# Kernel optimization log

Hardware: AMD Instinct MI355X
Metric: run time of the kernel (lower is better)

The kernel has to match this reference:

```python
import jax, jax.numpy as jnp
import numpy as np

B, N, K, D = 64, 1024, 512, 256  # batch, positions, codes, H*W


def setup_inputs() -> dict:
    key = jax.random.key(0)
    k1, k2 = jax.random.split(key)
    z_e_x = jax.random.normal(k1, (B, N, D), dtype=jnp.float32)
    # nn.Embedding(K, H*W) initialized uniform(-1/K, 1/K)
    codebook = jax.random.uniform(k2, (K, D), dtype=jnp.float32,
                                  minval=-1.0 / K, maxval=1.0 / K)
    return {"z_e_x": z_e_x, "codebook": codebook}


def _nearest_code(flat, codebook):
    # squared L2 distance via expansion: ||z||^2 - 2 z.e + ||e||^2
    d = ((flat * flat).sum(-1, keepdims=True)
         - 2.0 * flat @ codebook.T
         + (codebook * codebook).sum(-1))  # [M, K]
    return jnp.argmin(d, axis=-1)  # [M]


def reference(z_e_x, codebook):
    # Faithful to VQEmbedding.straight_through(z_e_x):
    #   z_q_x: quantized with straight-through estimator (grad -> z_e_x)
    #   z_q_x_bar: gather from live codebook (grad -> codebook)
    flat = z_e_x.reshape(-1, codebook.shape[1])  # [M, D]
    idx = _nearest_code(flat, jax.lax.stop_gradient(codebook))
    cb_sg = jax.lax.stop_gradient(codebook)
    z_q_st = flat + jax.lax.stop_gradient(cb_sg[idx] - flat)
    z_q_x = z_q_st.reshape(z_e_x.shape)
    z_q_x_bar = codebook[idx].reshape(z_e_x.shape)
    return z_q_x, z_q_x_bar
```

## Files before the change

### kernel.cpp

```cpp
#include <hip/hip_runtime.h>
#include <math.h>
#include <limits.h>

#define M_ROWS 65536
#define DD     256
#define KC     512
#define RPW    8
#define RPB    32

__device__ __forceinline__ float pw128_sq(const float4* __restrict__ q) {
  float r[8];
  {
    float4 a = q[0], b = q[1];
    r[0] = __fmul_rn(a.x, a.x); r[1] = __fmul_rn(a.y, a.y);
    r[2] = __fmul_rn(a.z, a.z); r[3] = __fmul_rn(a.w, a.w);
    r[4] = __fmul_rn(b.x, b.x); r[5] = __fmul_rn(b.y, b.y);
    r[6] = __fmul_rn(b.z, b.z); r[7] = __fmul_rn(b.w, b.w);
  }
#pragma unroll
  for (int i = 2; i < 32; i += 2) {
    float4 a = q[i], b = q[i + 1];
    r[0] = __fadd_rn(r[0], __fmul_rn(a.x, a.x));
    r[1] = __fadd_rn(r[1], __fmul_rn(a.y, a.y));
    r[2] = __fadd_rn(r[2], __fmul_rn(a.z, a.z));
    r[3] = __fadd_rn(r[3], __fmul_rn(a.w, a.w));
    r[4] = __fadd_rn(r[4], __fmul_rn(b.x, b.x));
    r[5] = __fadd_rn(r[5], __fmul_rn(b.y, b.y));
    r[6] = __fadd_rn(r[6], __fmul_rn(b.z, b.z));
    r[7] = __fadd_rn(r[7], __fmul_rn(b.w, b.w));
  }
  return __fadd_rn(__fadd_rn(__fadd_rn(r[0], r[1]), __fadd_rn(r[2], r[3])),
                   __fadd_rn(__fadd_rn(r[4], r[5]), __fadd_rn(r[6], r[7])));
}

__global__ void sumsq_kernel(const float* __restrict__ x, float* __restrict__ s,
                             int nrows) {
  int r = blockIdx.x * blockDim.x + threadIdx.x;
  if (r >= nrows) return;
  const float4* q = (const float4*)(x + (size_t)r * DD);
  s[r] = __fadd_rn(pw128_sq(q), pw128_sq(q + 32));
}

typedef __attribute__((address_space(1))) const void gas_void;
typedef __attribute__((address_space(3))) void las_void;
__device__ __forceinline__ void gl_lds16(const void* g, void* l) {
  __builtin_amdgcn_global_load_lds((gas_void*)g, (las_void*)l, 16, 0, 0);
}

__global__ __launch_bounds__(256) void vq_kernel(
    const float* __restrict__ z, const float* __restrict__ cb,
    const float* __restrict__ s, const float* __restrict__ se,
    float* __restrict__ out) {
  __shared__ float4 es4[KC * 4];
  __shared__ int best_l[RPB];

  const int tid = threadIdx.x;
  const int lane = tid & 63;
  const int wv = tid >> 6;
  const int rowbase =
      __builtin_amdgcn_readfirstlane((int)blockIdx.x * RPB + wv * RPW);
  const float4* zq = (const float4*)(z + (size_t)rowbase * DD);
  const float4* cg = (const float4*)cb;
  const int esw = (lane >> 1) & 3;

  float se_reg[8];
#pragma unroll
  for (int j = 0; j < 8; ++j) se_reg[j] = se[lane + 64 * j];

  float acc[8][8];
#pragma unroll
  for (int i = 0; i < 8; ++i)
#pragma unroll
    for (int j = 0; j < 8; ++j) acc[i][j] = 0.0f;

#pragma unroll 1
  for (int ks = 0; ks < 16; ++ks) {
#pragma unroll
    for (int seg = 0; seg < 8; ++seg) {
      int u = (wv * 8 + seg) * 64 + lane;
      int c = u >> 2;
      int q = (u & 3) ^ ((c >> 1) & 3);
      gl_lds16(&cg[(size_t)c * 64 + ks * 4 + q],
               (char*)es4 + (wv * 8 + seg) * 1024);
    }
    __syncthreads();

#pragma unroll
    for (int k4 = 0; k4 < 4; ++k4) {
      const float4* ep = &es4[lane * 4 + (k4 ^ esw)];
      float4 ef[8];
#pragma unroll
      for (int j = 0; j < 8; ++j) ef[j] = ep[j * 256];
#pragma unroll
      for (int i = 0; i < 8; ++i) {
        float4 zf = zq[(size_t)i * 64 + ks * 4 + k4];
#pragma unroll
        for (int j = 0; j < 8; ++j) {
          acc[i][j] = __fmaf_rn(zf.x, ef[j].x, acc[i][j]);
          acc[i][j] = __fmaf_rn(zf.y, ef[j].y, acc[i][j]);
          acc[i][j] = __fmaf_rn(zf.z, ef[j].z, acc[i][j]);
          acc[i][j] = __fmaf_rn(zf.w, ef[j].w, acc[i][j]);
        }
      }
    }
    __syncthreads();
  }

#pragma unroll
  for (int i = 0; i < 8; ++i) {
    float s_r = s[rowbase + i];
    float bd = INFINITY;
    int   bi = INT_MAX;
#pragma unroll
    for (int j = 0; j < 8; ++j) {
      int code = lane + 64 * j;
      float d = __fadd_rn(__fsub_rn(s_r, __fmul_rn(2.0f, acc[i][j])),
                          se_reg[j]);
      if (d < bd || (d == bd && code < bi)) { bd = d; bi = code; }
    }
#pragma unroll
    for (int off = 1; off < 64; off <<= 1) {
      float od = __shfl_xor(bd, off, 64);
      int   oi = __shfl_xor(bi, off, 64);
      if (od < bd || (od == bd && oi < bi)) { bd = od; bi = oi; }
    }
    if (lane == 0) best_l[wv * RPW + i] = bi;
  }
  __syncthreads();

  const int r0 = blockIdx.x * RPB;
  const float4* zg = (const float4*)z;
  float4* out0 = (float4*)out;
  float4* out1 = (float4*)(out + (size_t)M_ROWS * DD);
#pragma unroll
  for (int it = 0; it < 8; ++it) {
    int row = it * 4 + wv;
    size_t gidx = (size_t)(r0 + row) * 64 + lane;
    float4 zv = zg[gidx];
    float4 cv = cg[(size_t)best_l[row] * 64 + lane];
    float4 o0;
    o0.x = __fadd_rn(zv.x, __fsub_rn(cv.x, zv.x));
    o0.y = __fadd_rn(zv.y, __fsub_rn(cv.y, zv.y));
    o0.z = __fadd_rn(zv.z, __fsub_rn(cv.z, zv.z));
    o0.w = __fadd_rn(zv.w, __fsub_rn(cv.w, zv.w));
    out0[gidx] = o0;
    out1[gidx] = cv;
  }
}

extern "C" void kernel_launch(void* const* d_in, const int* in_sizes, int n_in,
                              void* d_out, int out_size, void* d_ws, size_t ws_size,
                              hipStream_t stream) {
  const float* z  = (const float*)d_in[0];
  const float* cb = (const float*)d_in[1];
  float* out = (float*)d_out;
  float* s  = (float*)d_ws;
  float* se = s + M_ROWS;

  sumsq_kernel<<<M_ROWS / 256, 256, 0, stream>>>(z, s, M_ROWS);
  sumsq_kernel<<<KC / 256, 256, 0, stream>>>(cb, se, KC);
  vq_kernel<<<M_ROWS / RPB, 256, 0, stream>>>(z, cb, s, se, out);
}
```

Measured before the change: 303.1 us.

## Double-buffer codebook LDS tiles and enlarge per-wave row tile in VQ kernel

Restructures the distance GEMM so each block has 8 waves of 16 rows each (128 rows per block) and stages codebook slices of 32 floats into double-buffered LDS. The next slice is loaded asynchronously while the current one is computed, which removes one barrier per step. Larger per-wave tiles cut codebook LDS traffic per FMA. The cost is higher register pressure (128 accumulators per lane) and 128 KB of LDS per block, which can lower occupancy and risks spills.

```diff
diff --git a/kernel.cpp b/kernel.cpp
--- a/kernel.cpp
+++ b/kernel.cpp
@@ -5,8 +5,10 @@
 #define M_ROWS 65536
 #define DD     256
 #define KC     512
-#define RPW    8
-#define RPB    32
+#define RPW    16
+#define WAVES  8
+#define RPB    (RPW * WAVES)
+#define KS     32
 
 __device__ __forceinline__ float pw128_sq(const float4* __restrict__ q) {
   float r[8];
@@ -47,11 +49,11 @@
   __builtin_amdgcn_global_load_lds((gas_void*)g, (las_void*)l, 16, 0, 0);
 }
 
-__global__ __launch_bounds__(256) void vq_kernel(
+__global__ __launch_bounds__(512) void vq_kernel(
     const float* __restrict__ z, const float* __restrict__ cb,
     const float* __restrict__ s, const float* __restrict__ se,
     float* __restrict__ out) {
-  __shared__ float4 es4[KC * 4];
+  __shared__ float4 es4[2][KC * 8];
   __shared__ int best_l[RPB];
 
   const int tid = threadIdx.x;
@@ -61,39 +63,39 @@
       __builtin_amdgcn_readfirstlane((int)blockIdx.x * RPB + wv * RPW);
   const float4* zq = (const float4*)(z + (size_t)rowbase * DD);
   const float4* cg = (const float4*)cb;
-  const int esw = (lane >> 1) & 3;
+  const int esw = lane & 7;
 
   float se_reg[8];
 #pragma unroll
   for (int j = 0; j < 8; ++j) se_reg[j] = se[lane + 64 * j];
 
-  float acc[8][8];
+  float acc[RPW][8];
 #pragma unroll
-  for (int i = 0; i < 8; ++i)
+  for (int i = 0; i < RPW; ++i)
 #pragma unroll
     for (int j = 0; j < 8; ++j) acc[i][j] = 0.0f;
 
-#pragma unroll 1
-  for (int ks = 0; ks < 16; ++ks) {
+  auto stage = [&](int b, int ks) {
 #pragma unroll
     for (int seg = 0; seg < 8; ++seg) {
-      int u = (wv * 8 + seg) * 64 + lane;
-      int c = u >> 2;
-      int q = (u & 3) ^ ((c >> 1) & 3);
-      gl_lds16(&cg[(size_t)c * 64 + ks * 4 + q],
-               (char*)es4 + (wv * 8 + seg) * 1024);
+      int u = seg * 512 + tid;
+      int c = u >> 3, qs = u & 7;
+      int q = qs ^ (c & 7);
+      gl_lds16(&cg[(size_t)c * 64 + ks * 8 + q],
+               (char*)&es4[b][0] + (size_t)(seg * 512 + wv * 64) * 16);
     }
-    __syncthreads();
+  };
 
+  auto compute = [&](int b, int ks) {
 #pragma unroll
-    for (int k4 = 0; k4 < 4; ++k4) {
-      const float4* ep = &es4[lane * 4 + (k4 ^ esw)];
+    for (int k4 = 0; k4 < 8; ++k4) {
+      const float4* ep = &es4[b][lane * 8 + (k4 ^ esw)];
       float4 ef[8];
 #pragma unroll
-      for (int j = 0; j < 8; ++j) ef[j] = ep[j * 256];
+      for (int j = 0; j < 8; ++j) ef[j] = ep[j * 512];
 #pragma unroll
-      for (int i = 0; i < 8; ++i) {
-        float4 zf = zq[(size_t)i * 64 + ks * 4 + k4];
+      for (int i = 0; i < RPW; ++i) {
+        float4 zf = zq[(size_t)i * 64 + ks * 8 + k4];
 #pragma unroll
         for (int j = 0; j < 8; ++j) {
           acc[i][j] = __fmaf_rn(zf.x, ef[j].x, acc[i][j]);
@@ -103,11 +105,21 @@
         }
       }
     }
+  };
+
+  stage(0, 0);
+  __syncthreads();
+  int b = 0;
+#pragma unroll 1
+  for (int ks = 0; ks < DD / KS; ++ks) {
+    if (ks < DD / KS - 1) stage(b ^ 1, ks + 1);
+    compute(b, ks);
     __syncthreads();
+    b ^= 1;
   }
 
 #pragma unroll
-  for (int i = 0; i < 8; ++i) {
+  for (int i = 0; i < RPW; ++i) {
     float s_r = s[rowbase + i];
     float bd = INFINITY;
     int   bi = INT_MAX;
@@ -133,11 +145,12 @@
   float4* out0 = (float4*)out;
   float4* out1 = (float4*)(out + (size_t)M_ROWS * DD);
 #pragma unroll
-  for (int it = 0; it < 8; ++it) {
-    int row = it * 4 + wv;
-    size_t gidx = (size_t)(r0 + row) * 64 + lane;
+  for (int it = 0; it < (RPB * 64) / 512; ++it) {
+    int u = it * 512 + tid;
+    int row = u >> 6, c4 = u & 63;
+    size_t gidx = (size_t)(r0 + row) * 64 + c4;
     float4 zv = zg[gidx];
-    float4 cv = cg[(size_t)best_l[row] * 64 + lane];
+    float4 cv = cg[(size_t)best_l[row] * 64 + c4];
     float4 o0;
     o0.x = __fadd_rn(zv.x, __fsub_rn(cv.x, zv.x));
     o0.y = __fadd_rn(zv.y, __fsub_rn(cv.y, zv.y));
@@ -159,5 +172,5 @@
 
   sumsq_kernel<<<M_ROWS / 256, 256, 0, stream>>>(z, s, M_ROWS);
   sumsq_kernel<<<KC / 256, 256, 0, stream>>>(cb, se, KC);
-  vq_kernel<<<M_ROWS / RPB, 256, 0, stream>>>(z, cb, s, se, out);
+  vq_kernel<<<M_ROWS / RPB, 512, 0, stream>>>(z, cb, s, se, out);
 }
```

Measured after the change: 425.3 us. 40.3% more time.

## Prefilter nearest codes with bf16 MFMA, then rescore candidates in fp32

Applied to the files above, without the earlier changes.

Replaces the single fp32 FMA distance kernel with a two-stage search. A bf16 MFMA pass computes approximate distances (the codebook norm is folded in as an extra K-slice) and keeps every code within an error-bound threshold of the row minimum. A second kernel rescores up to 32 candidates per row exactly in fp32, falling back to a full scan when more survive. This moves the bulk of the distance arithmetic onto matrix cores, at the cost of extra launches, a candidate buffer, and reliance on a heuristic threshold to keep exact argmin semantics.

```diff
diff --git a/kernel.cpp b/kernel.cpp
--- a/kernel.cpp
+++ b/kernel.cpp
@@ -5,8 +5,15 @@
 #define M_ROWS 65536
 #define DD     256
 #define KC     512
-#define RPW    8
-#define RPB    32
+#define CAP    32
+
+typedef __attribute__((ext_vector_type(8))) short bf16x8;
+typedef __attribute__((ext_vector_type(4))) float f32x4;
+
+__device__ __forceinline__ unsigned short bf16rne(float f) {
+  unsigned u = __float_as_uint(f);
+  return (unsigned short)((u + 0x7FFFu + ((u >> 16) & 1u)) >> 16);
+}
 
 __device__ __forceinline__ float pw128_sq(const float4* __restrict__ q) {
   float r[8];
@@ -47,105 +54,191 @@
   __builtin_amdgcn_global_load_lds((gas_void*)g, (las_void*)l, 16, 0, 0);
 }
 
-__global__ __launch_bounds__(256) void vq_kernel(
+__global__ void build_img_kernel(const float* __restrict__ cb,
+                                 const float* __restrict__ se,
+                                 unsigned short* __restrict__ img) {
+  int u0 = blockIdx.x * 256 + threadIdx.x;
+  if (u0 >= 9 * KC * 4) return;
+  int x = u0 & 3, c = (u0 >> 2) & (KC - 1), s = u0 >> 11;
+  int u = x ^ ((c >> 1) & 3);
+  unsigned short o[8];
+  if (s < 8) {
+    const float* src = cb + (size_t)c * DD + s * 32 + u * 8;
+#pragma unroll
+    for (int j = 0; j < 8; ++j) o[j] = bf16rne(src[j]);
+  } else {
+#pragma unroll
+    for (int j = 0; j < 8; ++j) o[j] = 0;
+    if (u == 0) o[0] = bf16rne(se[c]);
+  }
+  uint4 w;
+  w.x = (unsigned)o[0] | ((unsigned)o[1] << 16);
+  w.y = (unsigned)o[2] | ((unsigned)o[3] << 16);
+  w.z = (unsigned)o[4] | ((unsigned)o[5] << 16);
+  w.w = (unsigned)o[6] | ((unsigned)o[7] << 16);
+  *(uint4*)(img + (size_t)u0 * 8) = w;
+}
+
+__global__ __launch_bounds__(256) void filter_kernel(
+    const float* __restrict__ z, const unsigned short* __restrict__ img,
+    const float* __restrict__ s, int* __restrict__ cnt_g,
+    unsigned short* __restrict__ cands) {
+  __shared__ unsigned short b_lds[KC * 32];
+  __shared__ int cnt_lds[64];
+
+  const int tid = threadIdx.x;
+  const int lane = tid & 63, wv = tid >> 6;
+  const int lx = lane & 15, g = lane >> 4;
+  const int rowbase = blockIdx.x * 64;
+
+  if (tid < 64) cnt_lds[tid] = 0;
+
+  bf16x8 afrag[9];
+  {
+    const float* zrow = z + (size_t)(rowbase + wv * 16 + lx) * DD;
+#pragma unroll
+    for (int s8 = 0; s8 < 8; ++s8) {
+      const float4* p = (const float4*)(zrow + s8 * 32 + g * 8);
+      float4 x0 = p[0], x1 = p[1];
+      bf16x8 a;
+      a[0] = (short)bf16rne(-2.0f * x0.x); a[1] = (short)bf16rne(-2.0f * x0.y);
+      a[2] = (short)bf16rne(-2.0f * x0.z); a[3] = (short)bf16rne(-2.0f * x0.w);
+      a[4] = (short)bf16rne(-2.0f * x1.x); a[5] = (short)bf16rne(-2.0f * x1.y);
+      a[6] = (short)bf16rne(-2.0f * x1.z); a[7] = (short)bf16rne(-2.0f * x1.w);
+      afrag[s8] = a;
+    }
+    bf16x8 a;
+#pragma unroll
+    for (int j = 0; j < 8; ++j) a[j] = 0;
+    if (g == 0) a[0] = (short)0x3F80;
+    afrag[8] = a;
+  }
+
+  f32x4 acc[32];
+#pragma unroll
+  for (int t = 0; t < 32; ++t) acc[t] = (f32x4){0.f, 0.f, 0.f, 0.f};
+
+  const int bbase = lx * 4 + (g ^ ((lx >> 1) & 3));
+  const bf16x8* bunit = (const bf16x8*)b_lds;
+
+#pragma unroll
+  for (int ss = 0; ss < 9; ++ss) {
+    __syncthreads();
+#pragma unroll
+    for (int seg = 0; seg < 8; ++seg) {
+      gl_lds16((const char*)img + ((size_t)ss * 2048 + seg * 256 + tid) * 16,
+               (char*)b_lds + (seg * 256 + wv * 64) * 16);
+    }
+    __syncthreads();
+    bf16x8 av = afrag[ss];
+#pragma unroll
+    for (int t = 0; t < 32; ++t)
+      acc[t] = __builtin_amdgcn_mfma_f32_16x16x32_bf16(
+          av, bunit[t * 64 + bbase], acc[t], 0, 0, 0);
+  }
+
+  const unsigned long long gmask = 0xFFFFULL << (g * 16);
+  const unsigned long long below = (1ULL << lane) - 1;
+#pragma unroll
+  for (int q = 0; q < 4; ++q) {
+    float m = acc[0][q];
+#pragma unroll
+    for (int t = 1; t < 32; ++t) m = fminf(m, acc[t][q]);
+#pragma unroll
+    for (int off = 1; off < 16; off <<= 1)
+      m = fminf(m, __shfl_xor(m, off, 64));
+    const int r_loc = wv * 16 + 4 * g + q;
+    const float sr = s[rowbase + r_loc];
+    const float thr = m + 1.6e-3f * sqrtf(sr) + 1e-3f;
+#pragma unroll
+    for (int t = 0; t < 32; ++t) {
+      bool keep = (acc[t][q] <= thr);
+      unsigned long long mask = __ballot(keep);
+      if (keep) {
+        unsigned long long mym = mask & gmask;
+        int prefix = __popcll(mym & below);
+        unsigned long long lowbit = mym & (0ULL - mym);
+        int low = __popcll(lowbit - 1);
+        int base = 0;
+        if (lane == low) base = atomicAdd(&cnt_lds[r_loc], __popcll(mym));
+        base = __shfl(base, low, 64);
+        int off2 = base + prefix;
+        if (off2 < CAP)
+          cands[(size_t)(rowbase + r_loc) * CAP + off2] =
+              (unsigned short)(t * 16 + lx);
+      }
+    }
+  }
+  __syncthreads();
+  if (tid < 64) cnt_g[rowbase + tid] = cnt_lds[tid];
+}
+
+__global__ __launch_bounds__(256) void rescore_kernel(
     const float* __restrict__ z, const float* __restrict__ cb,
     const float* __restrict__ s, const float* __restrict__ se,
+    const int* __restrict__ cnt_g, const unsigned short* __restrict__ cands,
     float* __restrict__ out) {
-  __shared__ float4 es4[KC * 4];
-  __shared__ int best_l[RPB];
-
   const int tid = threadIdx.x;
-  const int lane = tid & 63;
-  const int wv = tid >> 6;
-  const int rowbase =
-      __builtin_amdgcn_readfirstlane((int)blockIdx.x * RPB + wv * RPW);
-  const float4* zq = (const float4*)(z + (size_t)rowbase * DD);
-  const float4* cg = (const float4*)cb;
-  const int esw = (lane >> 1) & 3;
-
-  float se_reg[8];
-#pragma unroll
-  for (int j = 0; j < 8; ++j) se_reg[j] = se[lane + 64 * j];
-
-  float acc[8][8];
-#pragma unroll
-  for (int i = 0; i < 8; ++i)
-#pragma unroll
-    for (int j = 0; j < 8; ++j) acc[i][j] = 0.0f;
-
+  const int lane = tid & 63, wv = tid >> 6;
+  const int r = blockIdx.x * 4 + wv;
+  const float4* zr = (const float4*)(z + (size_t)r * DD);
+  const float s_r = s[r];
+  const int cnt = cnt_g[r];
+  float bd = INFINITY;
+  int bi = INT_MAX;
+
+  if (cnt <= CAP) {
+    const bool act = lane < cnt;
+    const int code = act ? (int)cands[(size_t)r * CAP + lane] : 0;
+    const float4* cr = (const float4*)(cb + (size_t)code * DD);
+    float a = 0.0f;
+#pragma unroll 8
+    for (int k4 = 0; k4 < 64; ++k4) {
+      float4 zf = zr[k4], cf = cr[k4];
+      a = __fmaf_rn(zf.x, cf.x, a);
+      a = __fmaf_rn(zf.y, cf.y, a);
+      a = __fmaf_rn(zf.z, cf.z, a);
+      a = __fmaf_rn(zf.w, cf.w, a);
+    }
+    float d = __fadd_rn(__fsub_rn(s_r, __fmul_rn(2.0f, a)), se[code]);
+    if (act) { bd = d; bi = code; }
+  } else {
 #pragma unroll 1
-  for (int ks = 0; ks < 16; ++ks) {
-#pragma unroll
-    for (int seg = 0; seg < 8; ++seg) {
-      int u = (wv * 8 + seg) * 64 + lane;
-      int c = u >> 2;
-      int q = (u & 3) ^ ((c >> 1) & 3);
-      gl_lds16(&cg[(size_t)c * 64 + ks * 4 + q],
-               (char*)es4 + (wv * 8 + seg) * 1024);
-    }
-    __syncthreads();
-
-#pragma unroll
-    for (int k4 = 0; k4 < 4; ++k4) {
-      const float4* ep = &es4[lane * 4 + (k4 ^ esw)];
-      float4 ef[8];
-#pragma unroll
-      for (int j = 0; j < 8; ++j) ef[j] = ep[j * 256];
-#pragma unroll
-      for (int i = 0; i < 8; ++i) {
-        float4 zf = zq[(size_t)i * 64 + ks * 4 + k4];
-#pragma unroll
-        for (int j = 0; j < 8; ++j) {
-          acc[i][j] = __fmaf_rn(zf.x, ef[j].x, acc[i][j]);
-          acc[i][j] = __fmaf_rn(zf.y, ef[j].y, acc[i][j]);
-          acc[i][j] = __fmaf_rn(zf.z, ef[j].z, acc[i][j]);
-          acc[i][j] = __fmaf_rn(zf.w, ef[j].w, acc[i][j]);
-        }
-      }
-    }
-    __syncthreads();
-  }
-
-#pragma unroll
-  for (int i = 0; i < 8; ++i) {
-    float s_r = s[rowbase + i];
-    float bd = INFINITY;
-    int   bi = INT_MAX;
-#pragma unroll
     for (int j = 0; j < 8; ++j) {
       int code = lane + 64 * j;
-      float d = __fadd_rn(__fsub_rn(s_r, __fmul_rn(2.0f, acc[i][j])),
-                          se_reg[j]);
+      const float4* cr = (const float4*)(cb + (size_t)code * DD);
+      float a = 0.0f;
+#pragma unroll 4
+      for (int k4 = 0; k4 < 64; ++k4) {
+        float4 zf = zr[k4], cf = cr[k4];
+        a = __fmaf_rn(zf.x, cf.x, a);
+        a = __fmaf_rn(zf.y, cf.y, a);
+        a = __fmaf_rn(zf.z, cf.z, a);
+        a = __fmaf_rn(zf.w, cf.w, a);
+      }
+      float d = __fadd_rn(__fsub_rn(s_r, __fmul_rn(2.0f, a)), se[code]);
       if (d < bd || (d == bd && code < bi)) { bd = d; bi = code; }
     }
-#pragma unroll
-    for (int off = 1; off < 64; off <<= 1) {
-      float od = __shfl_xor(bd, off, 64);
-      int   oi = __shfl_xor(bi, off, 64);
-      if (od < bd || (od == bd && oi < bi)) { bd = od; bi = oi; }
-    }
-    if (lane == 0) best_l[wv * RPW + i] = bi;
-  }
-  __syncthreads();
-
-  const int r0 = blockIdx.x * RPB;
-  const float4* zg = (const float4*)z;
+  }
+#pragma unroll
+  for (int off = 1; off < 64; off <<= 1) {
+    float od = __shfl_xor(bd, off, 64);
+    int oi = __shfl_xor(bi, off, 64);
+    if (od < bd || (od == bd && oi < bi)) { bd = od; bi = oi; }
+  }
+  if (bi > KC - 1) bi = 0;
+
+  const float4* cbest = (const float4*)(cb + (size_t)bi * DD);
+  float4 zv = zr[lane], cv = cbest[lane];
+  float4 o0;
+  o0.x = __fadd_rn(zv.x, __fsub_rn(cv.x, zv.x));
+  o0.y = __fadd_rn(zv.y, __fsub_rn(cv.y, zv.y));
+  o0.z = __fadd_rn(zv.z, __fsub_rn(cv.z, zv.z));
+  o0.w = __fadd_rn(zv.w, __fsub_rn(cv.w, zv.w));
   float4* out0 = (float4*)out;
-  float4* out1 = (float4*)(out + (size_t)M_ROWS * DD);
-#pragma unroll
-  for (int it = 0; it < 8; ++it) {
-    int row = it * 4 + wv;
-    size_t gidx = (size_t)(r0 + row) * 64 + lane;
-    float4 zv = zg[gidx];
-    float4 cv = cg[(size_t)best_l[row] * 64 + lane];
-    float4 o0;
-    o0.x = __fadd_rn(zv.x, __fsub_rn(cv.x, zv.x));
-    o0.y = __fadd_rn(zv.y, __fsub_rn(cv.y, zv.y));
-    o0.z = __fadd_rn(zv.z, __fsub_rn(cv.z, zv.z));
-    o0.w = __fadd_rn(zv.w, __fsub_rn(cv.w, zv.w));
-    out0[gidx] = o0;
-    out1[gidx] = cv;
-  }
+  float4* out1 = out0 + (size_t)M_ROWS * 64;
+  out0[(size_t)r * 64 + lane] = o0;
+  out1[(size_t)r * 64 + lane] = cv;
 }
 
 extern "C" void kernel_launch(void* const* d_in, const int* in_sizes, int n_in,
@@ -154,10 +247,16 @@
   const float* z  = (const float*)d_in[0];
   const float* cb = (const float*)d_in[1];
   float* out = (float*)d_out;
+
   float* s  = (float*)d_ws;
   float* se = s + M_ROWS;
+  unsigned short* img = (unsigned short*)(se + KC);
+  int* cnt = (int*)((char*)d_ws + 559104);
+  unsigned short* cands = (unsigned short*)((char*)d_ws + 821248);
 
   sumsq_kernel<<<M_ROWS / 256, 256, 0, stream>>>(z, s, M_ROWS);
   sumsq_kernel<<<KC / 256, 256, 0, stream>>>(cb, se, KC);
-  vq_kernel<<<M_ROWS / RPB, 256, 0, stream>>>(z, cb, s, se, out);
-}
+  build_img_kernel<<<(9 * KC * 4 + 255) / 256, 256, 0, stream>>>(cb, se, img);
+  filter_kernel<<<M_ROWS / 64, 256, 0, stream>>>(z, img, s, cnt, cands);
+  rescore_kernel<<<M_ROWS / 4, 256, 0, stream>>>(z, cb, s, se, cnt, cands, out);
+}
```

Result: slower. 454.8 us, median of 4 (+50.0%).
